# Optimization experiments

Hardware: AMD Instinct MI355X
Metric: run time of the kernel (lower is better)

Reference implementation:

```python
import jax, jax.numpy as jnp
import numpy as np

N_NODES = 100000
N_EDGES = 1600000
N_CLIQUES = 250000
HIDDEN = 128
HEADS = 4
D_K = 32          # attention_ratio
ATT_DIM = HEADS * D_K  # 128


def setup_inputs() -> dict:
    key = jax.random.key(0)
    ks = jax.random.split(key, 12)
    x = jax.random.normal(ks[0], (N_NODES, HIDDEN), dtype=jnp.float32)
    edge_index = jax.random.randint(ks[1], (2, N_EDGES), 0, N_NODES)
    d0_index = jax.random.randint(ks[2], (2, 2 * N_EDGES), 0, N_NODES)
    twoClique_index = jax.random.randint(ks[3], (3, N_CLIQUES), 0, N_NODES)
    d1_index = jax.random.randint(ks[4], (2, 3 * N_CLIQUES), 0, N_EDGES)
    # learned params (torch nn.Linear uses W [out,in]; we store transposed [in,out])
    scale = 0.01
    Qw = jax.random.normal(ks[5], (HIDDEN, ATT_DIM), dtype=jnp.float32) * scale
    Qb = jax.random.normal(ks[6], (ATT_DIM,), dtype=jnp.float32) * scale
    Kw = jax.random.normal(ks[7], (HIDDEN, ATT_DIM), dtype=jnp.float32) * scale
    Kb = jax.random.normal(ks[8], (ATT_DIM,), dtype=jnp.float32) * scale
    Vw = jax.random.normal(ks[9], (HIDDEN, ATT_DIM), dtype=jnp.float32) * scale
    Vb = jax.random.normal(ks[10], (ATT_DIM,), dtype=jnp.float32) * scale
    return {"x": x, "edge_index": edge_index, "d0_index": d0_index,
            "twoClique_index": twoClique_index, "d1_index": d1_index,
            "Qw": Qw, "Qb": Qb, "Kw": Kw, "Kb": Kb, "Vw": Vw, "Vb": Vb}


def reference(x, edge_index, d0_index, twoClique_index, d1_index,
              Qw, Qb, Kw, Kb, Vw, Vb):
    # projections: [N, H, d_k]
    q = (x @ Qw + Qb).reshape(-1, HEADS, D_K)
    k = (x @ Kw + Kb).reshape(-1, HEADS, D_K)
    v = (x @ Vw + Vb).reshape(-1, HEADS, D_K)

    i, j, kk = twoClique_index[0], twoClique_index[1], twoClique_index[2]
    q_i, q_j, q_k = q[i], q[j], q[kk]
    k_i, k_j, k_k = k[i], k[j], k[kk]
    v_i, v_j, v_k = v[i], v[j], v[kk]

    # symmetrized 6-term contraction, sum over d_k then mean over heads
    pre = (q_i * k_j * v_k + q_j * k_k * v_i + q_k * k_i * v_j
           + q_j * k_i * v_k + q_k * k_j * v_i + q_i * k_k * v_j).sum(-1) * (1.0 / 6.0)
    pre = pre.mean(axis=-1)            # [nCliques]
    diagA2 = jnp.exp(pre)              # use_squareplus=False

    # clique -> edge: each clique contributes its score to its 3 edges
    clique_score_per_edge = jnp.repeat(diagA2, 3)           # [3*nCliques]
    diagA1 = jax.ops.segment_sum(clique_score_per_edge, d1_index[1],
                                 num_segments=edge_index.shape[1])

    # edge -> node: each edge contributes its score to its 2 endpoints
    edge_score_per_node = jnp.repeat(diagA1, 2)             # [2*nEdges]
    diagA0 = jax.ops.segment_sum(edge_score_per_node, d0_index[1],
                                 num_segments=N_NODES)
    return (diagA0, diagA1, diagA2)
```

## Files before the change

kernel.cpp:

```cpp
#include <hip/hip_runtime.h>

#define N_NODES   100000
#define N_EDGES   1600000
#define N_CLIQUES 250000

typedef unsigned short ushort8v __attribute__((ext_vector_type(8)));
typedef __bf16 bf16x8 __attribute__((ext_vector_type(8)));
typedef float f32x4 __attribute__((ext_vector_type(4)));
typedef float f32x2 __attribute__((ext_vector_type(2)));

__device__ __forceinline__ float bf2f(unsigned short u) {
    return __uint_as_float(((unsigned int)u) << 16);
}
__device__ __forceinline__ unsigned short f2bf(float f) {
    unsigned int u = __float_as_uint(f);
    u += 0x7FFFu + ((u >> 16) & 1u);
    return (unsigned short)(u >> 16);
}

__global__ __launch_bounds__(256) void prep_weights(
    const float* __restrict__ Qw, const float* __restrict__ Kw,
    const float* __restrict__ Vw, unsigned short* __restrict__ wt)
{
    int idx = blockIdx.x * 256 + threadIdx.x;
    int t = idx >> 14;
    int rem = idx & 16383;
    int col = rem >> 7;
    int k = rem & 127;
    const float* W = (t == 0) ? Qw : ((t == 1) ? Kw : Vw);
    wt[idx] = f2bf(W[k * 128 + col]);
}

#define CSTRIDE 132
__global__ __launch_bounds__(256, 4) void proj_mfma(
    const float* __restrict__ x,
    const unsigned short* __restrict__ wt,
    const float* __restrict__ Qb, const float* __restrict__ Kb,
    const float* __restrict__ Vb,
    unsigned char* __restrict__ qkv8)
{
    __shared__ unsigned short wS[128 * 128];
    __shared__ float biasS[128];

    const int tid  = threadIdx.x;
    const int lane = tid & 63;
    const int w    = tid >> 6;
    const int node0 = blockIdx.x * 64;
    const int arow = lane & 15;
    const int kg   = lane >> 4;

    bf16x8 afrag[4];
    const int myNode = node0 + w * 16 + arow;
    const bool valid = myNode < N_NODES;
    const float* xrow = x + (size_t)myNode * 128;
    #pragma unroll
    for (int kt = 0; kt < 4; ++kt) {
        float4 v0, v1;
        const int kbase = kt * 32 + kg * 8;
        if (valid) {
            v0 = *(const float4*)(xrow + kbase);
            v1 = *(const float4*)(xrow + kbase + 4);
        } else {
            v0.x = v0.y = v0.z = v0.w = 0.f;
            v1.x = v1.y = v1.z = v1.w = 0.f;
        }
        ushort8v u;
        u[0] = f2bf(v0.x); u[1] = f2bf(v0.y); u[2] = f2bf(v0.z); u[3] = f2bf(v0.w);
        u[4] = f2bf(v1.x); u[5] = f2bf(v1.y); u[6] = f2bf(v1.z); u[7] = f2bf(v1.w);
        afrag[kt] = __builtin_bit_cast(bf16x8, u);
    }

    for (int t = 0; t < 3; ++t) {
        __syncthreads();
        {
            const unsigned short* src = wt + t * 16384;
            #pragma unroll
            for (int it = 0; it < 8; ++it) {
                int i   = tid + it * 256;
                int col = i >> 4;
                int ko  = i & 15;
                *(ushort8v*)&wS[col * 128 + (ko ^ (col & 7)) * 8] =
                    *(const ushort8v*)(src + i * 8);
            }
            if (tid < 128) biasS[tid] = ((t == 0) ? Qb : ((t == 1) ? Kb : Vb))[tid];
        }
        __syncthreads();

        f32x4 acc[8];
        #pragma unroll
        for (int c = 0; c < 8; ++c) acc[c] = (f32x4){0.f, 0.f, 0.f, 0.f};

        #pragma unroll
        for (int kt = 0; kt < 4; ++kt) {
            const int chunk = kt * 4 + kg;
            #pragma unroll
            for (int c = 0; c < 8; ++c) {
                const int col = c * 16 + arow;
                ushort8v bu = *(const ushort8v*)&wS[col * 128 + (chunk ^ (col & 7)) * 8];
                acc[c] = __builtin_amdgcn_mfma_f32_16x16x32_bf16(
                    afrag[kt], __builtin_bit_cast(bf16x8, bu), acc[c], 0, 0, 0);
            }
        }
        __syncthreads();

        #pragma unroll
        for (int c = 0; c < 8; ++c) {
            const int col = c * 16 + arow;
            const float b = biasS[col];
            #pragma unroll
            for (int r = 0; r < 4; ++r) {
                const int orow = w * 16 + kg * 4 + r;
                wS[orow * CSTRIDE + col] = f2bf(acc[c][r] + b);
            }
        }
        __syncthreads();

        #pragma unroll
        for (int it = 0; it < 2; ++it) {
            int i    = tid + it * 256;
            int orow = i >> 3;
            int ch   = i & 7;
            int node = node0 + orow;
            if (node < N_NODES) {
                const unsigned short* src = &wS[orow * CSTRIDE + ch * 16];
                unsigned int wo[4];
                #pragma unroll
                for (int q = 0; q < 4; ++q) {
                    float f0 = bf2f(src[q * 4 + 0]);
                    float f1 = bf2f(src[q * 4 + 1]);
                    float f2 = bf2f(src[q * 4 + 2]);
                    float f3 = bf2f(src[q * 4 + 3]);
                    int lo = __builtin_amdgcn_cvt_pk_fp8_f32(f0, f1, 0, false);
                    wo[q] = (unsigned int)__builtin_amdgcn_cvt_pk_fp8_f32(f2, f3, lo, true);
                }
                uint4 o; o.x = wo[0]; o.y = wo[1]; o.z = wo[2]; o.w = wo[3];
                *(uint4*)(qkv8 + (size_t)node * 384 + t * 128 + ch * 16) = o;
            }
        }
    }
}

#define DEC4(w_, a_) { f32x2 lo_ = __builtin_amdgcn_cvt_pk_f32_fp8((int)(w_), false); \
                       f32x2 hi_ = __builtin_amdgcn_cvt_pk_f32_fp8((int)(w_), true);  \
                       a_[0] = lo_[0]; a_[1] = lo_[1]; a_[2] = hi_[0]; a_[3] = hi_[1]; }

__global__ __launch_bounds__(256) void clique_kernel(
    const unsigned char* __restrict__ qkv8,
    const int* __restrict__ tci,
    const int* __restrict__ d1row1,
    const int* __restrict__ d0row1,
    float* __restrict__ outA1,
    float* __restrict__ outA2,
    float* __restrict__ a0c)
{
    const int tid = threadIdx.x;
    const int lane8 = tid & 7;
    const int cliq = (blockIdx.x * 256 + tid) >> 3;
    if (cliq >= N_CLIQUES) return;

    const int ni = tci[cliq];
    const int nj = tci[N_CLIQUES + cliq];
    const int nk = tci[2 * N_CLIQUES + cliq];
    const int d0 = lane8 * 16;

    const unsigned char* bi = qkv8 + (size_t)ni * 384 + d0;
    const unsigned char* bj = qkv8 + (size_t)nj * 384 + d0;
    const unsigned char* bk = qkv8 + (size_t)nk * 384 + d0;

    const uint4 rQi = *(const uint4*)(bi);
    const uint4 rKi = *(const uint4*)(bi + 128);
    const uint4 rVi = *(const uint4*)(bi + 256);
    const uint4 rQj = *(const uint4*)(bj);
    const uint4 rKj = *(const uint4*)(bj + 128);
    const uint4 rVj = *(const uint4*)(bj + 256);
    const uint4 rQk = *(const uint4*)(bk);
    const uint4 rKk = *(const uint4*)(bk + 128);
    const uint4 rVk = *(const uint4*)(bk + 256);

    float s = 0.f;
    #pragma unroll
    for (int c = 0; c < 4; ++c) {
        unsigned int wQi = ((const unsigned int*)&rQi)[c];
        unsigned int wKi = ((const unsigned int*)&rKi)[c];
        unsigned int wVi = ((const unsigned int*)&rVi)[c];
        unsigned int wQj = ((const unsigned int*)&rQj)[c];
        unsigned int wKj = ((const unsigned int*)&rKj)[c];
        unsigned int wVj = ((const unsigned int*)&rVj)[c];
        unsigned int wQk = ((const unsigned int*)&rQk)[c];
        unsigned int wKk = ((const unsigned int*)&rKk)[c];
        unsigned int wVk = ((const unsigned int*)&rVk)[c];
        float qi_[4], ki_[4], vi_[4], qj_[4], kj_[4], vj_[4], qk_[4], kk_[4], vk_[4];
        DEC4(wQi, qi_); DEC4(wKi, ki_); DEC4(wVi, vi_);
        DEC4(wQj, qj_); DEC4(wKj, kj_); DEC4(wVj, vj_);
        DEC4(wQk, qk_); DEC4(wKk, kk_); DEC4(wVk, vk_);
        #pragma unroll
        for (int d = 0; d < 4; ++d) {
            s = fmaf(qi_[d], fmaf(kj_[d], vk_[d], kk_[d] * vj_[d]), s);
            s = fmaf(qj_[d], fmaf(kk_[d], vi_[d], ki_[d] * vk_[d]), s);
            s = fmaf(qk_[d], fmaf(ki_[d], vj_[d], kj_[d] * vi_[d]), s);
        }
    }
    s += __shfl_xor(s, 1);
    s += __shfl_xor(s, 2);
    s += __shfl_xor(s, 4);

    float score = expf(s * (1.0f / 24.0f));
    if (lane8 == 0) outA2[cliq] = score;
    if (lane8 < 3) {
        int e = d1row1[3 * cliq + lane8];
        atomicAdd(outA1 + e, score);
        int2 tg = *(const int2*)(d0row1 + 2 * (size_t)e);
        float* base = a0c + (size_t)(cliq & 7) * N_NODES;
        atomicAdd(base + tg.x, score);
        atomicAdd(base + tg.y, score);
    }
}

__global__ __launch_bounds__(256) void combineA0_kernel(
    const float* __restrict__ a0c, float* __restrict__ outA0)
{
    int n = blockIdx.x * 256 + threadIdx.x;
    if (n < N_NODES) {
        float s = 0.f;
        #pragma unroll
        for (int c = 0; c < 8; ++c) s += a0c[(size_t)c * N_NODES + n];
        outA0[n] = s;
    }
}

extern "C" void kernel_launch(void* const* d_in, const int* in_sizes, int n_in,
                              void* d_out, int out_size, void* d_ws, size_t ws_size,
                              hipStream_t stream)
{
    const float* x  = (const float*)d_in[0];
    const int*   d0i = (const int*)d_in[2];
    const int*   tci = (const int*)d_in[3];
    const int*   d1i = (const int*)d_in[4];
    const float* Qw = (const float*)d_in[5];
    const float* Qb = (const float*)d_in[6];
    const float* Kw = (const float*)d_in[7];
    const float* Kb = (const float*)d_in[8];
    const float* Vw = (const float*)d_in[9];
    const float* Vb = (const float*)d_in[10];

    const int* d0row1 = d0i + 2 * (size_t)N_EDGES;
    const int* d1row1 = d1i + 3 * (size_t)N_CLIQUES;

    const size_t QKV_B = (size_t)N_NODES * 384;
    const size_t WT_B  = 3 * 128 * 128 * 2;
    unsigned char* qkv8 = (unsigned char*)d_ws;
    unsigned short* wt  = (unsigned short*)(qkv8 + QKV_B);
    float* a0c = (float*)(qkv8 + QKV_B + WT_B);

    float* outA0 = (float*)d_out;
    float* outA1 = outA0 + N_NODES;
    float* outA2 = outA0 + N_NODES + N_EDGES;

    hipMemsetAsync(outA1, 0, (size_t)N_EDGES * 4, stream);
    hipMemsetAsync(a0c, 0, (size_t)8 * N_NODES * 4, stream);
    prep_weights<<<192, 256, 0, stream>>>(Qw, Kw, Vw, wt);
    proj_mfma<<<(N_NODES + 63) / 64, 256, 0, stream>>>(x, wt, Qb, Kb, Vb, qkv8);
    clique_kernel<<<(N_CLIQUES * 8 + 255) / 256, 256, 0, stream>>>(
        qkv8, tci, d1row1, d0row1, outA1, outA2, a0c);
    combineA0_kernel<<<(N_NODES + 255) / 256, 256, 0, stream>>>(a0c, outA0);
}
```

Baseline: 165.7 us.

## Keep projection weights in registers with persistent grid-stride node tiles

The projection kernel now splits the 384 QKV output columns across the four waves, with each wave holding its 96-column slice of bf16 weights and bias in registers for the whole kernel. A persistent grid of 1024 blocks walks 16-node tiles, so the per-block LDS weight staging and most block barriers go away. Each wave stages its outputs in a small private LDS stripe before packing them to fp8. The cost is high register pressure from 24 weight fragments per lane, which may lower occupancy, and every wave in a block now reloads the same x tile.

```diff
diff --git a/kernel.cpp b/kernel.cpp
--- a/kernel.cpp
+++ b/kernel.cpp
@@ -31,110 +31,90 @@
     wt[idx] = f2bf(W[k * 128 + col]);
 }
 
-#define CSTRIDE 132
-__global__ __launch_bounds__(256, 4) void proj_mfma(
+__global__ __launch_bounds__(256) void proj_reg(
     const float* __restrict__ x,
     const unsigned short* __restrict__ wt,
     const float* __restrict__ Qb, const float* __restrict__ Kb,
     const float* __restrict__ Vb,
     unsigned char* __restrict__ qkv8)
 {
-    __shared__ unsigned short wS[128 * 128];
-    __shared__ float biasS[128];
+    __shared__ unsigned short stripeS[4][16][104];
 
     const int tid  = threadIdx.x;
     const int lane = tid & 63;
     const int w    = tid >> 6;
-    const int node0 = blockIdx.x * 64;
     const int arow = lane & 15;
     const int kg   = lane >> 4;
 
-    bf16x8 afrag[4];
-    const int myNode = node0 + w * 16 + arow;
-    const bool valid = myNode < N_NODES;
-    const float* xrow = x + (size_t)myNode * 128;
+    bf16x8 bfrag[6][4];
+    float biasr[6];
     #pragma unroll
-    for (int kt = 0; kt < 4; ++kt) {
-        float4 v0, v1;
-        const int kbase = kt * 32 + kg * 8;
-        if (valid) {
-            v0 = *(const float4*)(xrow + kbase);
-            v1 = *(const float4*)(xrow + kbase + 4);
-        } else {
-            v0.x = v0.y = v0.z = v0.w = 0.f;
-            v1.x = v1.y = v1.z = v1.w = 0.f;
-        }
-        ushort8v u;
-        u[0] = f2bf(v0.x); u[1] = f2bf(v0.y); u[2] = f2bf(v0.z); u[3] = f2bf(v0.w);
-        u[4] = f2bf(v1.x); u[5] = f2bf(v1.y); u[6] = f2bf(v1.z); u[7] = f2bf(v1.w);
-        afrag[kt] = __builtin_bit_cast(bf16x8, u);
-    }
-
-    for (int t = 0; t < 3; ++t) {
-        __syncthreads();
-        {
-            const unsigned short* src = wt + t * 16384;
+    for (int c = 0; c < 6; ++c) {
+        int g = w * 96 + c * 16 + arow;
+        int t = g >> 7, col = g & 127;
+        const float* Bp = (t == 0) ? Qb : ((t == 1) ? Kb : Vb);
+        biasr[c] = Bp[col];
+        #pragma unroll
+        for (int kt = 0; kt < 4; ++kt)
+            bfrag[c][kt] = __builtin_bit_cast(bf16x8,
+                *(const ushort8v*)(wt + t * 16384 + col * 128 + kt * 32 + kg * 8));
+    }
+
+    for (int tile = blockIdx.x; tile < N_NODES / 16; tile += gridDim.x) {
+        const float* xr = x + ((size_t)tile * 16 + arow) * 128;
+        bf16x8 afrag[4];
+        #pragma unroll
+        for (int kt = 0; kt < 4; ++kt) {
+            float4 v0 = *(const float4*)(xr + kt * 32 + kg * 8);
+            float4 v1 = *(const float4*)(xr + kt * 32 + kg * 8 + 4);
+            ushort8v u;
+            u[0] = f2bf(v0.x); u[1] = f2bf(v0.y); u[2] = f2bf(v0.z); u[3] = f2bf(v0.w);
+            u[4] = f2bf(v1.x); u[5] = f2bf(v1.y); u[6] = f2bf(v1.z); u[7] = f2bf(v1.w);
+            afrag[kt] = __builtin_bit_cast(bf16x8, u);
+        }
+
+        f32x4 acc[6];
+        #pragma unroll
+        for (int c = 0; c < 6; ++c) acc[c] = (f32x4){0.f, 0.f, 0.f, 0.f};
+        #pragma unroll
+        for (int kt = 0; kt < 4; ++kt)
             #pragma unroll
-            for (int it = 0; it < 8; ++it) {
-                int i   = tid + it * 256;
-                int col = i >> 4;
-                int ko  = i & 15;
-                *(ushort8v*)&wS[col * 128 + (ko ^ (col & 7)) * 8] =
-                    *(const ushort8v*)(src + i * 8);
-            }
-            if (tid < 128) biasS[tid] = ((t == 0) ? Qb : ((t == 1) ? Kb : Vb))[tid];
-        }
-        __syncthreads();
-
-        f32x4 acc[8];
-        #pragma unroll
-        for (int c = 0; c < 8; ++c) acc[c] = (f32x4){0.f, 0.f, 0.f, 0.f};
-
-        #pragma unroll
-        for (int kt = 0; kt < 4; ++kt) {
-            const int chunk = kt * 4 + kg;
+            for (int c = 0; c < 6; ++c)
+                acc[c] = __builtin_amdgcn_mfma_f32_16x16x32_bf16(
+                    afrag[kt], bfrag[c][kt], acc[c], 0, 0, 0);
+
+        #pragma unroll
+        for (int c = 0; c < 6; ++c) {
+            const float b = biasr[c];
             #pragma unroll
-            for (int c = 0; c < 8; ++c) {
-                const int col = c * 16 + arow;
-                ushort8v bu = *(const ushort8v*)&wS[col * 128 + (chunk ^ (col & 7)) * 8];
-                acc[c] = __builtin_amdgcn_mfma_f32_16x16x32_bf16(
-                    afrag[kt], __builtin_bit_cast(bf16x8, bu), acc[c], 0, 0, 0);
-            }
-        }
-        __syncthreads();
-
-        #pragma unroll
-        for (int c = 0; c < 8; ++c) {
-            const int col = c * 16 + arow;
-            const float b = biasS[col];
-            #pragma unroll
-            for (int r = 0; r < 4; ++r) {
-                const int orow = w * 16 + kg * 4 + r;
-                wS[orow * CSTRIDE + col] = f2bf(acc[c][r] + b);
-            }
-        }
-        __syncthreads();
+            for (int r = 0; r < 4; ++r)
+                stripeS[w][kg * 4 + r][c * 16 + arow] = f2bf(acc[c][r] + b);
+        }
+        asm volatile("s_waitcnt lgkmcnt(0)" ::: "memory");
 
         #pragma unroll
         for (int it = 0; it < 2; ++it) {
-            int i    = tid + it * 256;
-            int orow = i >> 3;
-            int ch   = i & 7;
-            int node = node0 + orow;
-            if (node < N_NODES) {
-                const unsigned short* src = &wS[orow * CSTRIDE + ch * 16];
+            int i = lane + it * 64;
+            if (i < 96) {
+                int row = i / 6, ch = i % 6;
+                int g0 = w * 96 + ch * 16;
+                int t = g0 >> 7, col0 = g0 & 127;
+                const unsigned short* sp = &stripeS[w][row][ch * 16];
+                ushort8v b0 = *(const ushort8v*)sp;
+                ushort8v b1 = *(const ushort8v*)(sp + 8);
                 unsigned int wo[4];
-                #pragma unroll
-                for (int q = 0; q < 4; ++q) {
-                    float f0 = bf2f(src[q * 4 + 0]);
-                    float f1 = bf2f(src[q * 4 + 1]);
-                    float f2 = bf2f(src[q * 4 + 2]);
-                    float f3 = bf2f(src[q * 4 + 3]);
-                    int lo = __builtin_amdgcn_cvt_pk_fp8_f32(f0, f1, 0, false);
-                    wo[q] = (unsigned int)__builtin_amdgcn_cvt_pk_fp8_f32(f2, f3, lo, true);
+                {
+                    int lo0 = __builtin_amdgcn_cvt_pk_fp8_f32(bf2f(b0[0]), bf2f(b0[1]), 0, false);
+                    wo[0] = (unsigned int)__builtin_amdgcn_cvt_pk_fp8_f32(bf2f(b0[2]), bf2f(b0[3]), lo0, true);
+                    int lo1 = __builtin_amdgcn_cvt_pk_fp8_f32(bf2f(b0[4]), bf2f(b0[5]), 0, false);
+                    wo[1] = (unsigned int)__builtin_amdgcn_cvt_pk_fp8_f32(bf2f(b0[6]), bf2f(b0[7]), lo1, true);
+                    int lo2 = __builtin_amdgcn_cvt_pk_fp8_f32(bf2f(b1[0]), bf2f(b1[1]), 0, false);
+                    wo[2] = (unsigned int)__builtin_amdgcn_cvt_pk_fp8_f32(bf2f(b1[2]), bf2f(b1[3]), lo2, true);
+                    int lo3 = __builtin_amdgcn_cvt_pk_fp8_f32(bf2f(b1[4]), bf2f(b1[5]), 0, false);
+                    wo[3] = (unsigned int)__builtin_amdgcn_cvt_pk_fp8_f32(bf2f(b1[6]), bf2f(b1[7]), lo3, true);
                 }
                 uint4 o; o.x = wo[0]; o.y = wo[1]; o.z = wo[2]; o.w = wo[3];
-                *(uint4*)(qkv8 + (size_t)node * 384 + t * 128 + ch * 16) = o;
+                *(uint4*)(qkv8 + ((size_t)tile * 16 + row) * 384 + t * 128 + col0) = o;
             }
         }
     }
@@ -259,7 +239,7 @@
     hipMemsetAsync(outA1, 0, (size_t)N_EDGES * 4, stream);
     hipMemsetAsync(a0c, 0, (size_t)8 * N_NODES * 4, stream);
     prep_weights<<<192, 256, 0, stream>>>(Qw, Kw, Vw, wt);
-    proj_mfma<<<(N_NODES + 63) / 64, 256, 0, stream>>>(x, wt, Qb, Kb, Vb, qkv8);
+    proj_reg<<<1024, 256, 0, stream>>>(x, wt, Qb, Kb, Vb, qkv8);
     clique_kernel<<<(N_CLIQUES * 8 + 255) / 256, 256, 0, stream>>>(
         qkv8, tci, d1row1, d0row1, outA1, outA2, a0c);
     combineA0_kernel<<<(N_NODES + 255) / 256, 256, 0, stream>>>(a0c, outA0);
```

Measured after the change: 182.5 us. 1.1x slower.
